# Kernel tuning notes

Hardware: AMD Instinct MI355X
Metric: run time of the kernel (lower is better)

The kernel has to match this reference:

```python
import jax, jax.numpy as jnp
import numpy as np

N_NODES = 100000
N_EDGES = 1600000
IN_CH, HID_CH, LAT = 32, 32, 16


def _gcn_layer(h, W, b, src, dst, norm):
    # PyG GCNConv: h' = scatter_add(norm * (h W)[src] -> dst) + b
    h = h @ W                                   # [N, out]
    msg = h[src] * norm[:, None]                # [E+N, out] gather
    out = jax.ops.segment_sum(msg, dst, num_segments=N_NODES)
    return out + b


def setup_inputs() -> dict:
    key = jax.random.key(0)
    ks = jax.random.split(key, 8)
    x = jax.random.normal(ks[0], (N_NODES, IN_CH), dtype=jnp.float32)
    edge_index = jax.random.randint(ks[1], (2, N_EDGES), 0, N_NODES, dtype=jnp.int32)
    def glorot(k, fan_in, fan_out):
        lim = np.sqrt(6.0 / (fan_in + fan_out)).astype(np.float32)
        return jax.random.uniform(k, (fan_in, fan_out), jnp.float32, -lim, lim)
    return {
        "x": x,
        "edge_index": edge_index,
        "W1": glorot(ks[2], IN_CH, HID_CH),
        "b1": jnp.zeros((HID_CH,), jnp.float32),
        "Wmu": glorot(ks[3], HID_CH, LAT),
        "bmu": jnp.zeros((LAT,), jnp.float32),
        "Wlv": glorot(ks[4], HID_CH, LAT),
        "blv": jnp.zeros((LAT,), jnp.float32),
    }


def reference(x, edge_index, W1, b1, Wmu, bmu, Wlv, blv):
    # Add self-loops (GCNConv default add_self_loops=True)
    loops = jnp.arange(N_NODES, dtype=edge_index.dtype)
    src = jnp.concatenate([edge_index[0], loops])
    dst = jnp.concatenate([edge_index[1], loops])
    # Symmetric normalization: deg over destinations, norm = d^-1/2[src] * d^-1/2[dst]
    deg = jax.ops.segment_sum(jnp.ones_like(dst, dtype=x.dtype), dst,
                              num_segments=N_NODES)
    dinv = jnp.where(deg > 0, jax.lax.rsqrt(deg), 0.0)
    norm = dinv[src] * dinv[dst]                # [E+N]

    h = jax.nn.relu(_gcn_layer(x, W1, b1, src, dst, norm))
    mu = _gcn_layer(h, Wmu, bmu, src, dst, norm)
    logvar = _gcn_layer(h, Wlv, blv, src, dst, norm)
    return (mu, logvar)
```

## Files before the change

### kernel.cpp

```cpp
#include <hip/hip_runtime.h>
#include <hip/hip_fp16.h>

#define N_NODES 100000
#define N_EDGES 1600000
#define NCB 98
#define CAPC 17500
#define P1_CHUNK 4096
#define P1_BLOCKS 391
#define BK 64
#define NBF 1563
#define CAPF 1408
#define P2_SPLIT 16


__global__ __launch_bounds__(512) void k_part1(const int* __restrict__ src,
                                               const int* __restrict__ dst,
                                               int* __restrict__ cursor1,
                                               unsigned* __restrict__ packed1) {
    __shared__ int bh[NCB];
    __shared__ int base[NCB];
    int t = threadIdx.x;
    if (t < NCB) bh[t] = 0;
    __syncthreads();
    int e0 = blockIdx.x * P1_CHUNK;
    int e1 = e0 + P1_CHUNK; if (e1 > N_EDGES) e1 = N_EDGES;
    for (int e = e0 + t; e < e1; e += 512)
        atomicAdd(&bh[((unsigned)dst[e]) >> 10], 1);
    __syncthreads();
    if (t < NCB) {
        int c = bh[t];
        base[t] = t * CAPC + ((c > 0) ? atomicAdd(&cursor1[t], c) : 0);
        bh[t] = 0;
    }
    __syncthreads();
    for (int e = e0 + t; e < e1; e += 512) {
        unsigned d = (unsigned)dst[e];
        int b = d >> 10;
        int r = atomicAdd(&bh[b], 1);
        int pos = base[b] + r;
        if (pos < (b + 1) * CAPC)
            packed1[pos] = ((d & 1023u) << 17) | (unsigned)src[e];
    }
}

__global__ __launch_bounds__(256) void k_part2(const unsigned* __restrict__ packed1,
                                               const int* __restrict__ cursor1,
                                               int* __restrict__ cursor2,
                                               unsigned* __restrict__ packed2) {
    __shared__ int bh[16];
    __shared__ int base[16];
    int t = threadIdx.x;
    int c = blockIdx.x / P2_SPLIT;
    int k = blockIdx.x % P2_SPLIT;
    int cc = cursor1[c]; if (cc > CAPC) cc = CAPC;
    int s0 = c * CAPC + (k * cc) / P2_SPLIT;
    int s1 = c * CAPC + ((k + 1) * cc) / P2_SPLIT;
    if (t < 16) bh[t] = 0;
    __syncthreads();
    for (int i = s0 + t; i < s1; i += 256)
        atomicAdd(&bh[(packed1[i] >> 17) >> 6], 1);
    __syncthreads();
    if (t < 16) {
        int cnt = bh[t];
        int fb = c * 16 + t;
        base[t] = fb * CAPF + ((cnt > 0) ? atomicAdd(&cursor2[fb], cnt) : 0);
        bh[t] = 0;
    }
    __syncthreads();
    for (int i = s0 + t; i < s1; i += 256) {
        unsigned pk = packed1[i];
        unsigned dl = pk >> 17;
        int f = dl >> 6;
        int r = atomicAdd(&bh[f], 1);
        int pos = base[f] + r;
        int fb = c * 16 + f;
        if (pos < (fb + 1) * CAPF)
            packed2[pos] = ((dl & 63u) << 17) | (pk & 0x1FFFFu);
    }
}

__global__ __launch_bounds__(256) void k_csrx(const unsigned* __restrict__ packed2,
                                              const int* __restrict__ cursor2,
                                              const float* __restrict__ x,
                                              const float* __restrict__ W1,
                                              int* __restrict__ rowBeg,
                                              int* __restrict__ rowEnd,
                                              float* __restrict__ dinv,
                                              int* __restrict__ srcSorted,
                                              __half* __restrict__ p1) {
    __shared__ int cnt[BK];
    __shared__ int scn[BK];
    __shared__ int cur[BK];
    __shared__ float sW[1024];
    int t = threadIdx.x;
    int b = blockIdx.x;
    int seg0 = b * CAPF;
    int cc = cursor2[b]; if (cc > CAPF) cc = CAPF;
    int segEnd = seg0 + cc;
    if (t < BK) cnt[t] = 0;
    for (int i = t; i < 1024; i += 256) sW[i] = W1[i];
    __syncthreads();
    for (int i = seg0 + t; i < segEnd; i += 256)
        atomicAdd(&cnt[packed2[i] >> 17], 1);
    __syncthreads();
    int v = (t < BK) ? cnt[t] : 0;
    if (t < BK) scn[t] = v;
    __syncthreads();
    for (int off = 1; off < BK; off <<= 1) {
        int u = (t < BK && t >= off) ? scn[t - off] : 0;
        __syncthreads();
        if (t < BK) scn[t] += u;
        __syncthreads();
    }
    int node = b * BK + t;
    if (t < BK) {
        int start = seg0 + scn[t] - v;
        if (node < N_NODES) {
            rowBeg[node] = start;
            rowEnd[node] = start + v;
            dinv[node] = rsqrtf((float)(v + 1));
        }
        cur[t] = start;
    }
    __syncthreads();
    for (int i = seg0 + t; i < segEnd; i += 256) {
        unsigned pk = packed2[i];
        int pos = atomicAdd(&cur[pk >> 17], 1);
        srcSorted[pos] = (int)(pk & 0x1FFFFu);
    }
    int lane = t & 31;
    for (int r = (t >> 5); r < BK; r += 8) {
        int nd = b * BK + r;
        if (nd > N_NODES) break;
        if (nd == N_NODES) {
            p1[nd * 32 + lane] = __float2half(0.f);
            continue;
        }
        float xv = x[nd * 32 + lane];
        float a = 0.f;
#pragma unroll
        for (int k = 0; k < 32; ++k) {
            float xk = __shfl(xv, k, 32);
            a += xk * sW[k * 32 + lane];
        }
        float di = rsqrtf((float)(cnt[r] + 1));
        p1[nd * 32 + lane] = __float2half(di * a);
    }
}

__device__ __forceinline__ __half2 h2of(const float4& v, int c) {
    return reinterpret_cast<const __half2*>(&v)[c];
}

__device__ __forceinline__ void gatherRow4(const int* __restrict__ srcSorted,
                                           const float4* __restrict__ P,
                                           int beg, int end, int l,
                                           float* __restrict__ acc ) {
    for (int base = beg; base < end; base += 8) {
        int i0 = base + l, i1 = base + 4 + l;
        int sA = (i0 < end) ? srcSorted[i0] : N_NODES;
        int sB = (i1 < end) ? srcSorted[i1] : N_NODES;
        float4 v0 = P[__shfl(sA, 0, 4) * 4 + l];
        float4 v1 = P[__shfl(sA, 1, 4) * 4 + l];
        float4 v2 = P[__shfl(sA, 2, 4) * 4 + l];
        float4 v3 = P[__shfl(sA, 3, 4) * 4 + l];
        float4 v4 = P[__shfl(sB, 0, 4) * 4 + l];
        float4 v5 = P[__shfl(sB, 1, 4) * 4 + l];
        float4 v6 = P[__shfl(sB, 2, 4) * 4 + l];
        float4 v7 = P[__shfl(sB, 3, 4) * 4 + l];
#pragma unroll
        for (int c = 0; c < 4; ++c) {
            __half2 s01 = __hadd2(h2of(v0, c), h2of(v1, c));
            __half2 s23 = __hadd2(h2of(v2, c), h2of(v3, c));
            __half2 s45 = __hadd2(h2of(v4, c), h2of(v5, c));
            __half2 s67 = __hadd2(h2of(v6, c), h2of(v7, c));
            __half2 sum = __hadd2(__hadd2(s01, s23), __hadd2(s45, s67));
            float2 f = __half22float2(sum);
            acc[2 * c]     += f.x;
            acc[2 * c + 1] += f.y;
        }
    }
}

__global__ __launch_bounds__(256) void k_gx2(const int* __restrict__ rowBeg,
                                             const int* __restrict__ rowEnd,
                                             const int* __restrict__ srcSorted,
                                             const __half* __restrict__ p1,
                                             const float* __restrict__ dinv,
                                             const float* __restrict__ b1,
                                             const float* __restrict__ Wmu,
                                             const float* __restrict__ Wlv,
                                             __half* __restrict__ p2) {
    __shared__ float sW[1024];
    __shared__ float sB[32];
    int t = threadIdx.x;
    for (int i = t; i < 1024; i += 256) {
        int k = i >> 5, oc = i & 31;
        sW[i] = (oc < 16) ? Wmu[k * 16 + oc] : Wlv[k * 16 + (oc - 16)];
    }
    if (t < 32) sB[t] = b1[t];
    __syncthreads();
    int l = t & 3;
    int node = blockIdx.x * 64 + (t >> 2);
    if (node > N_NODES) return;
    const float4* P = (const float4*)p1;
    if (node == N_NODES) {
        ((float4*)p2)[node * 4 + l] = make_float4(0.f, 0.f, 0.f, 0.f);
        return;
    }
    float acc[8] = {0.f, 0.f, 0.f, 0.f, 0.f, 0.f, 0.f, 0.f};
    gatherRow4(srcSorted, P, rowBeg[node], rowEnd[node], l, acc);
    float di = dinv[node];
    float4 ps = P[node * 4 + l];
    float h[8];
#pragma unroll
    for (int c = 0; c < 4; ++c) {
        float2 f = __half22float2(h2of(ps, c));
        h[2 * c]     = fmaxf(di * (acc[2 * c]     + f.x) + sB[8 * l + 2 * c],     0.f);
        h[2 * c + 1] = fmaxf(di * (acc[2 * c + 1] + f.y) + sB[8 * l + 2 * c + 1], 0.f);
    }
    float o[8] = {0.f, 0.f, 0.f, 0.f, 0.f, 0.f, 0.f, 0.f};
    const float4* W4 = (const float4*)sW;
#pragma unroll
    for (int m = 0; m < 4; ++m) {
#pragma unroll
        for (int j = 0; j < 8; ++j) {
            float hk = __shfl(h[j], m, 4);
            int k = 8 * m + j;
            float4 wa = W4[k * 8 + 2 * l];
            float4 wb = W4[k * 8 + 2 * l + 1];
            o[0] += hk * wa.x; o[1] += hk * wa.y; o[2] += hk * wa.z; o[3] += hk * wa.w;
            o[4] += hk * wb.x; o[5] += hk * wb.y; o[6] += hk * wb.z; o[7] += hk * wb.w;
        }
    }
    __half2 r0 = __floats2half2_rn(di * o[0], di * o[1]);
    __half2 r1 = __floats2half2_rn(di * o[2], di * o[3]);
    __half2 r2 = __floats2half2_rn(di * o[4], di * o[5]);
    __half2 r3 = __floats2half2_rn(di * o[6], di * o[7]);
    float4 st;
    st.x = *reinterpret_cast<float*>(&r0);
    st.y = *reinterpret_cast<float*>(&r1);
    st.z = *reinterpret_cast<float*>(&r2);
    st.w = *reinterpret_cast<float*>(&r3);
    ((float4*)p2)[node * 4 + l] = st;
}

__global__ __launch_bounds__(256) void k_gfin(const int* __restrict__ rowBeg,
                                              const int* __restrict__ rowEnd,
                                              const int* __restrict__ srcSorted,
                                              const __half* __restrict__ p2,
                                              const float* __restrict__ dinv,
                                              const float* __restrict__ bmu,
                                              const float* __restrict__ blv,
                                              float* __restrict__ out) {
    __shared__ float sB[32];
    int t = threadIdx.x;
    if (t < 32) sB[t] = (t < 16) ? bmu[t] : blv[t - 16];
    __syncthreads();
    int l = t & 3;
    int node = blockIdx.x * 64 + (t >> 2);
    if (node >= N_NODES) return;
    const float4* P = (const float4*)p2;
    float acc[8] = {0.f, 0.f, 0.f, 0.f, 0.f, 0.f, 0.f, 0.f};
    gatherRow4(srcSorted, P, rowBeg[node], rowEnd[node], l, acc);
    float di = dinv[node];
    float4 ps = P[node * 4 + l];
    float v[8];
#pragma unroll
    for (int c = 0; c < 4; ++c) {
        float2 f = __half22float2(h2of(ps, c));
        v[2 * c]     = di * (acc[2 * c]     + f.x) + sB[8 * l + 2 * c];
        v[2 * c + 1] = di * (acc[2 * c + 1] + f.y) + sB[8 * l + 2 * c + 1];
    }
    float4 o0 = make_float4(v[0], v[1], v[2], v[3]);
    float4 o1 = make_float4(v[4], v[5], v[6], v[7]);
    float4* dst4 = (l < 2) ? (float4*)out
                           : (float4*)(out + (size_t)N_NODES * 16);
    int b4 = node * 4 + (l & 1) * 2;
    dst4[b4]     = o0;
    dst4[b4 + 1] = o1;
}

extern "C" void kernel_launch(void* const* d_in, const int* in_sizes, int n_in,
                              void* d_out, int out_size, void* d_ws, size_t ws_size,
                              hipStream_t stream) {
    const float* x   = (const float*)d_in[0];
    const int*   ei  = (const int*)d_in[1];
    const float* W1  = (const float*)d_in[2];
    const float* b1  = (const float*)d_in[3];
    const float* Wmu = (const float*)d_in[4];
    const float* bmu = (const float*)d_in[5];
    const float* Wlv = (const float*)d_in[6];
    const float* blv = (const float*)d_in[7];
    float* out = (float*)d_out;

    const int* src = ei;
    const int* dst = ei + N_EDGES;

    size_t off = 0;
    int* cursor1 = (int*)d_ws;                          off += NCB;
    int* cursor2 = (int*)d_ws + off;                    off += NBF;
    int* rowBeg  = (int*)d_ws + off;                    off += N_NODES;
    int* rowEnd  = (int*)d_ws + off;                    off += N_NODES;
    float* dinv  = (float*)((int*)d_ws + off);          off += N_NODES;
    off = (off + 63) & ~(size_t)63;
    unsigned* packed1 = (unsigned*)((int*)d_ws + off);  off += (size_t)NCB * CAPC;
    off = (off + 63) & ~(size_t)63;
    unsigned* packed2 = (unsigned*)((int*)d_ws + off);  off += (size_t)NBF * CAPF;
    off = (off + 63) & ~(size_t)63;
    int* srcSorted    = (int*)d_ws + off;
    __half* p1h       = (__half*)packed1;
    __half* p2h       = (__half*)packed2;

    hipMemsetAsync(d_ws, 0, (size_t)(NCB + NBF) * sizeof(int), stream);
    k_part1<<<P1_BLOCKS, 512, 0, stream>>>(src, dst, cursor1, packed1);
    k_part2<<<NCB * P2_SPLIT, 256, 0, stream>>>(packed1, cursor1, cursor2, packed2);
    k_csrx <<<NBF, 256, 0, stream>>>(packed2, cursor2, x, W1,
                                     rowBeg, rowEnd, dinv, srcSorted, p1h);
    k_gx2  <<<NBF, 256, 0, stream>>>(rowBeg, rowEnd, srcSorted, p1h, dinv,
                                     b1, Wmu, Wlv, p2h);
    k_gfin <<<NBF, 256, 0, stream>>>(rowBeg, rowEnd, srcSorted, p2h, dinv,
                                     bmu, blv, out);
}
```

Measured before the change: 190.6 us.

## Replace two-pass radix partition with single 256-node bucket pass

Removes the second partition kernel by binning edges directly into 391 buckets of 256 destination nodes, so the CSR build kernel sorts each bucket locally with 512 threads. The partition kernel now preloads eight src/dst pairs per thread into registers instead of reading dst twice and src once. This drops one launch and a full read/write of the packed edge array. In exchange there are fewer, larger CSR blocks, which lowers parallelism in that stage and puts more shared-atomic contention on the bucket counters.

```diff
diff --git a/kernel.cpp b/kernel.cpp
--- a/kernel.cpp
+++ b/kernel.cpp
@@ -3,14 +3,12 @@
 
 #define N_NODES 100000
 #define N_EDGES 1600000
-#define NCB 98
-#define CAPC 17500
+#define NCB 391
+#define CAPC 4736
 #define P1_CHUNK 4096
 #define P1_BLOCKS 391
-#define BK 64
-#define NBF 1563
-#define CAPF 1408
-#define P2_SPLIT 16
+#define BKN 256
+#define NBF_G 1563
 
 
 __global__ __launch_bounds__(512) void k_part1(const int* __restrict__ src,
@@ -24,8 +22,15 @@
     __syncthreads();
     int e0 = blockIdx.x * P1_CHUNK;
     int e1 = e0 + P1_CHUNK; if (e1 > N_EDGES) e1 = N_EDGES;
-    for (int e = e0 + t; e < e1; e += 512)
-        atomicAdd(&bh[((unsigned)dst[e]) >> 10], 1);
+    int d[8], s[8];
+#pragma unroll
+    for (int j = 0; j < 8; ++j) {
+        int e = e0 + t + j * 512;
+        if (e < e1) { d[j] = dst[e]; s[j] = src[e]; } else d[j] = -1;
+    }
+#pragma unroll
+    for (int j = 0; j < 8; ++j)
+        if (d[j] >= 0) atomicAdd(&bh[((unsigned)d[j]) >> 8], 1);
     __syncthreads();
     if (t < NCB) {
         int c = bh[t];
@@ -33,54 +38,20 @@
         bh[t] = 0;
     }
     __syncthreads();
-    for (int e = e0 + t; e < e1; e += 512) {
-        unsigned d = (unsigned)dst[e];
-        int b = d >> 10;
+#pragma unroll
+    for (int j = 0; j < 8; ++j) {
+        if (d[j] < 0) continue;
+        unsigned dd = (unsigned)d[j];
+        int b = dd >> 8;
         int r = atomicAdd(&bh[b], 1);
         int pos = base[b] + r;
         if (pos < (b + 1) * CAPC)
-            packed1[pos] = ((d & 1023u) << 17) | (unsigned)src[e];
-    }
-}
-
-__global__ __launch_bounds__(256) void k_part2(const unsigned* __restrict__ packed1,
-                                               const int* __restrict__ cursor1,
-                                               int* __restrict__ cursor2,
-                                               unsigned* __restrict__ packed2) {
-    __shared__ int bh[16];
-    __shared__ int base[16];
-    int t = threadIdx.x;
-    int c = blockIdx.x / P2_SPLIT;
-    int k = blockIdx.x % P2_SPLIT;
-    int cc = cursor1[c]; if (cc > CAPC) cc = CAPC;
-    int s0 = c * CAPC + (k * cc) / P2_SPLIT;
-    int s1 = c * CAPC + ((k + 1) * cc) / P2_SPLIT;
-    if (t < 16) bh[t] = 0;
-    __syncthreads();
-    for (int i = s0 + t; i < s1; i += 256)
-        atomicAdd(&bh[(packed1[i] >> 17) >> 6], 1);
-    __syncthreads();
-    if (t < 16) {
-        int cnt = bh[t];
-        int fb = c * 16 + t;
-        base[t] = fb * CAPF + ((cnt > 0) ? atomicAdd(&cursor2[fb], cnt) : 0);
-        bh[t] = 0;
-    }
-    __syncthreads();
-    for (int i = s0 + t; i < s1; i += 256) {
-        unsigned pk = packed1[i];
-        unsigned dl = pk >> 17;
-        int f = dl >> 6;
-        int r = atomicAdd(&bh[f], 1);
-        int pos = base[f] + r;
-        int fb = c * 16 + f;
-        if (pos < (fb + 1) * CAPF)
-            packed2[pos] = ((dl & 63u) << 17) | (pk & 0x1FFFFu);
-    }
-}
-
-__global__ __launch_bounds__(256) void k_csrx(const unsigned* __restrict__ packed2,
-                                              const int* __restrict__ cursor2,
+            packed1[pos] = ((dd & 255u) << 17) | (unsigned)s[j];
+    }
+}
+
+__global__ __launch_bounds__(512) void k_csrx(const unsigned* __restrict__ packed1,
+                                              const int* __restrict__ cursor1,
                                               const float* __restrict__ x,
                                               const float* __restrict__ W1,
                                               int* __restrict__ rowBeg,
@@ -88,32 +59,32 @@
                                               float* __restrict__ dinv,
                                               int* __restrict__ srcSorted,
                                               __half* __restrict__ p1) {
-    __shared__ int cnt[BK];
-    __shared__ int scn[BK];
-    __shared__ int cur[BK];
+    __shared__ int cnt[BKN];
+    __shared__ int scn[BKN];
+    __shared__ int cur[BKN];
     __shared__ float sW[1024];
     int t = threadIdx.x;
     int b = blockIdx.x;
-    int seg0 = b * CAPF;
-    int cc = cursor2[b]; if (cc > CAPF) cc = CAPF;
+    int seg0 = b * CAPC;
+    int cc = cursor1[b]; if (cc > CAPC) cc = CAPC;
     int segEnd = seg0 + cc;
-    if (t < BK) cnt[t] = 0;
-    for (int i = t; i < 1024; i += 256) sW[i] = W1[i];
-    __syncthreads();
-    for (int i = seg0 + t; i < segEnd; i += 256)
-        atomicAdd(&cnt[packed2[i] >> 17], 1);
-    __syncthreads();
-    int v = (t < BK) ? cnt[t] : 0;
-    if (t < BK) scn[t] = v;
-    __syncthreads();
-    for (int off = 1; off < BK; off <<= 1) {
-        int u = (t < BK && t >= off) ? scn[t - off] : 0;
+    if (t < BKN) cnt[t] = 0;
+    for (int i = t; i < 1024; i += 512) sW[i] = W1[i];
+    __syncthreads();
+    for (int i = seg0 + t; i < segEnd; i += 512)
+        atomicAdd(&cnt[packed1[i] >> 17], 1);
+    __syncthreads();
+    int v = (t < BKN) ? cnt[t] : 0;
+    if (t < BKN) scn[t] = v;
+    __syncthreads();
+    for (int off = 1; off < BKN; off <<= 1) {
+        int u = (t < BKN && t >= off) ? scn[t - off] : 0;
         __syncthreads();
-        if (t < BK) scn[t] += u;
+        if (t < BKN) scn[t] += u;
         __syncthreads();
     }
-    int node = b * BK + t;
-    if (t < BK) {
+    int node = b * BKN + t;
+    if (t < BKN) {
         int start = seg0 + scn[t] - v;
         if (node < N_NODES) {
             rowBeg[node] = start;
@@ -123,14 +94,14 @@
         cur[t] = start;
     }
     __syncthreads();
-    for (int i = seg0 + t; i < segEnd; i += 256) {
-        unsigned pk = packed2[i];
+    for (int i = seg0 + t; i < segEnd; i += 512) {
+        unsigned pk = packed1[i];
         int pos = atomicAdd(&cur[pk >> 17], 1);
         srcSorted[pos] = (int)(pk & 0x1FFFFu);
     }
     int lane = t & 31;
-    for (int r = (t >> 5); r < BK; r += 8) {
-        int nd = b * BK + r;
+    for (int r = (t >> 5); r < BKN; r += 16) {
+        int nd = b * BKN + r;
         if (nd > N_NODES) break;
         if (nd == N_NODES) {
             p1[nd * 32 + lane] = __float2half(0.f);
@@ -299,26 +270,24 @@
 
     size_t off = 0;
     int* cursor1 = (int*)d_ws;                          off += NCB;
-    int* cursor2 = (int*)d_ws + off;                    off += NBF;
     int* rowBeg  = (int*)d_ws + off;                    off += N_NODES;
     int* rowEnd  = (int*)d_ws + off;                    off += N_NODES;
     float* dinv  = (float*)((int*)d_ws + off);          off += N_NODES;
     off = (off + 63) & ~(size_t)63;
     unsigned* packed1 = (unsigned*)((int*)d_ws + off);  off += (size_t)NCB * CAPC;
     off = (off + 63) & ~(size_t)63;
-    unsigned* packed2 = (unsigned*)((int*)d_ws + off);  off += (size_t)NBF * CAPF;
-    off = (off + 63) & ~(size_t)63;
-    int* srcSorted    = (int*)d_ws + off;
-    __half* p1h       = (__half*)packed1;
-    __half* p2h       = (__half*)packed2;
-
-    hipMemsetAsync(d_ws, 0, (size_t)(NCB + NBF) * sizeof(int), stream);
+    int* srcSorted    = (int*)d_ws + off;               off += (size_t)NCB * CAPC;
+    off = (off + 63) & ~(size_t)63;
+    __half* p1h = (__half*)((int*)d_ws + off);          off += (size_t)(N_NODES + 1) * 16;
+    off = (off + 63) & ~(size_t)63;
+    __half* p2h = (__half*)((int*)d_ws + off);
+
+    hipMemsetAsync(d_ws, 0, (size_t)NCB * sizeof(int), stream);
     k_part1<<<P1_BLOCKS, 512, 0, stream>>>(src, dst, cursor1, packed1);
-    k_part2<<<NCB * P2_SPLIT, 256, 0, stream>>>(packed1, cursor1, cursor2, packed2);
-    k_csrx <<<NBF, 256, 0, stream>>>(packed2, cursor2, x, W1,
+    k_csrx <<<NCB, 512, 0, stream>>>(packed1, cursor1, x, W1,
                                      rowBeg, rowEnd, dinv, srcSorted, p1h);
-    k_gx2  <<<NBF, 256, 0, stream>>>(rowBeg, rowEnd, srcSorted, p1h, dinv,
-                                     b1, Wmu, Wlv, p2h);
-    k_gfin <<<NBF, 256, 0, stream>>>(rowBeg, rowEnd, srcSorted, p2h, dinv,
-                                     bmu, blv, out);
-}
+    k_gx2  <<<NBF_G, 256, 0, stream>>>(rowBeg, rowEnd, srcSorted, p1h, dinv,
+                                       b1, Wmu, Wlv, p2h);
+    k_gfin <<<NBF_G, 256, 0, stream>>>(rowBeg, rowEnd, srcSorted, p2h, dinv,
+                                       bmu, blv, out);
+}
```

Measured after the change: 188.0 us. No clear change (-1.4%).
